# Performance work log

Hardware: AMD Instinct MI355X
Metric: run time of the kernel (lower is better)

## Reference

```python
import jax, jax.numpy as jnp
import numpy as np

# Config constants (mirroring repo globals C.*)
B, L, D = 128, 200, 256          # batch, history length, d_model
NT = 10000                        # num_types (items)
NU = 50000                        # C.USER_NUMBER
NL = 4                            # n_layers
BETA_1 = 0.1                      # C.BETA_1


def _l2norm(x, eps):
    n = jnp.linalg.norm(x, axis=-1, keepdims=True)
    return x / jnp.maximum(n, eps)


def setup_inputs() -> dict:
    key = jax.random.key(0)
    ks = jax.random.split(key, 7)
    user_id = jax.random.randint(ks[0], (B,), 1, NU)
    event_type = jax.random.randint(ks[1], (B, L), 1, NT + 1)  # 1..NT (non-pad)
    adjacent_matrix = jax.random.uniform(ks[2], (NT, NT), jnp.float32)
    pop_encoding = jax.random.normal(ks[3], (NT + 1, D), jnp.float32) * 0.02
    event_emb_w = (jax.random.normal(ks[4], (NT + 1, D), jnp.float32) * 0.02).at[0].set(0.0)
    user_emb_w = (jax.random.normal(ks[5], (NU, D), jnp.float32) * 0.02).at[0].set(0.0)
    layer_ws = jax.random.normal(ks[6], (NL, D, D), jnp.float32) * 0.05
    return {"user_id": user_id, "event_type": event_type,
            "adjacent_matrix": adjacent_matrix, "pop_encoding": pop_encoding,
            "event_emb_w": event_emb_w, "user_emb_w": user_emb_w,
            "layer_ws": layer_ws}


def reference(user_id, event_type, adjacent_matrix, pop_encoding,
              event_emb_w, user_emb_w, layer_ws):
    # non-pad mask (pad idx = 0)
    non_pad = (event_type != 0).astype(jnp.float32)[..., None]  # (B,L,1)

    enc = event_emb_w[event_type]                 # (B,L,D)
    user = user_emb_w[user_id]                    # (B,D)
    pop = pop_encoding[event_type] * non_pad      # (B,L,D)

    # user-specific disentanglement: enc += sign(enc) * normalize(user)
    enc = enc + jnp.sign(enc) * _l2norm(user, 1e-12)[:, None, :]

    # batched adjacency gather: adj[b] = A[e-1][:, e-1] + A[e-1, e-1] (row-broadcast)
    idx = event_type - 1                          # (B,L)
    adj = adjacent_matrix[idx[:, :, None], idx[:, None, :]]      # (B,L,L)
    adj = adj + adjacent_matrix[idx, idx][:, None, :]            # diag broadcast over rows

    # hGCN layer stack: x <- leaky_relu((adj @ x) @ W)
    for i in range(NL):
        enc = jax.nn.leaky_relu(jnp.einsum('bls,bsd->bld', adj, enc) @ layer_ws[i])

    output = enc.mean(axis=1)                     # (B,D)
    user_embeddings = jnp.concatenate([output, pop.mean(axis=1) * BETA_1], axis=-1)  # (B,2D)

    # Predictor (evaluation=True path)
    item_encoding = event_emb_w[1:]               # (NT,D)
    out = user_embeddings[:, :D] @ item_encoding.T  # (B,NT)
    out = _l2norm(out, 1e-5)
    prediction = jnp.tanh(out)
    return prediction, user_embeddings, pop
```

## Files before the change

### kernel.cpp

```cpp
#include <hip/hip_runtime.h>
#include <math.h>

#define B_ 128
#define L_ 200
#define D_ 256
#define NT_ 10000
#define NL_ 4
#define BETA1 0.1f

typedef _Float16 f16x8 __attribute__((ext_vector_type(8)));
typedef _Float16 f16x4 __attribute__((ext_vector_type(4)));
typedef _Float16 f16x2 __attribute__((ext_vector_type(2)));
typedef float f32x4 __attribute__((ext_vector_type(4)));

__device__ __forceinline__ void split2(float v, _Float16& h, _Float16& l) {
    h = (_Float16)v;
    l = (_Float16)(v - (float)h);
}

struct HL { _Float16 h, l; };
__device__ __forceinline__ HL split2v(float v) {
    HL r;
    r.h = (_Float16)v;
    r.l = (_Float16)(v - (float)r.h);
    return r;
}

__device__ __forceinline__ float getscale(const unsigned int* amax, int i, int extra) {
    float am = fmaxf(__uint_as_float(amax[i]), 1e-30f);
    return scalbnf(1.f, 6 - ilogbf(am) - extra);
}

__global__ void user_norm_kernel(const int* __restrict__ user_id,
                                 const float* __restrict__ user_emb_w,
                                 float* __restrict__ unorm,
                                 unsigned int* __restrict__ amax) {
    int b = blockIdx.x;
    int d = threadIdx.x;
    if (b == 0 && d < 16) amax[d] = 0u;
    int uid = user_id[b];
    float v = user_emb_w[(long)uid * D_ + d];
    float sq = v * v;
    for (int off = 32; off > 0; off >>= 1) sq += __shfl_down(sq, off, 64);
    __shared__ float s[4];
    int wid = d >> 6, lane = d & 63;
    if (lane == 0) s[wid] = sq;
    __syncthreads();
    float n = sqrtf(s[0] + s[1] + s[2] + s[3]);
    n = fmaxf(n, 1e-12f);
    unorm[b * D_ + d] = v / n;
}

__global__ void enc0pop_kernel(const int* __restrict__ event_type,
                               const float* __restrict__ E,
                               const float* __restrict__ pope,
                               const float* __restrict__ unorm,
                               float* __restrict__ encF,
                               float* __restrict__ pop_out,
                               unsigned int* __restrict__ amax) {
    int d = threadIdx.x;
    float m = 0.f;
    for (int bl = blockIdx.x; bl < B_ * L_; bl += gridDim.x) {
        int b = bl / L_;
        int et = event_type[bl];
        float e = E[(long)et * D_ + d];
        float sg = (e > 0.f) ? 1.f : ((e < 0.f) ? -1.f : 0.f);
        float u = unorm[b * D_ + d];
        float v = e + sg * u;
        encF[(long)bl * D_ + d] = v;
        m = fmaxf(m, fabsf(v));
        pop_out[(long)bl * D_ + d] = (et != 0) ? pope[(long)et * D_ + d] : 0.f;
    }
    for (int off = 32; off > 0; off >>= 1) m = fmaxf(m, __shfl_down(m, off, 64));
    __shared__ float sm[4];
    int wid = d >> 6, lane = d & 63;
    if (lane == 0) sm[wid] = m;
    __syncthreads();
    if (d == 0)
        atomicMax(amax, __float_as_uint(fmaxf(fmaxf(sm[0], sm[1]), fmaxf(sm[2], sm[3]))));
}

__global__ void diag_kernel(const int* __restrict__ event_type,
                            const float* __restrict__ A,
                            float* __restrict__ diag) {
    int i = blockIdx.x * blockDim.x + threadIdx.x;
    if (i >= B_ * L_) return;
    long idx = (long)event_type[i] - 1;
    diag[i] = A[idx * NT_ + idx];
}

__global__ void adj_split_kernel(const int* __restrict__ event_type,
                                 const float* __restrict__ A,
                                 const float* __restrict__ diag,
                                 _Float16* __restrict__ adjH,
                                 _Float16* __restrict__ adjL) {
    int b = blockIdx.y;
    int i0 = blockIdx.x * 4;
    int j = threadIdx.x;
    __shared__ int sidx[L_];
    __shared__ float sdiag[L_];
    if (j < L_) {
        sidx[j]  = event_type[b * L_ + j] - 1;
        sdiag[j] = diag[b * L_ + j];
    }
    __syncthreads();
    if (j >= L_) return;
    float dj = sdiag[j];
    int cj = sidx[j];
#pragma unroll
    for (int r = 0; r < 4; r++) {
        int i = i0 + r;
        float v = A[(long)sidx[i] * NT_ + cj] + dj;
        HL s = split2v(v);
        long o = ((long)b * L_ + i) * L_ + j;
        adjH[o] = s.h; adjL[o] = s.l;
    }
}

__global__ void wsplit_kernel(const float* __restrict__ W,
                              _Float16* __restrict__ WTh,
                              _Float16* __restrict__ WTl) {
    int layer = blockIdx.z;
    int k0 = blockIdx.y * 64, n0 = blockIdx.x * 64;
    const float* Wl = W + (long)layer * D_ * D_;
    __shared__ float t[64][65];
    int tid = threadIdx.x;
    for (int i = 0; i < 16; i++) {
        int idx = i * 256 + tid;
        int k = idx >> 6, n = idx & 63;
        t[k][n] = Wl[(long)(k0 + k) * D_ + n0 + n];
    }
    __syncthreads();
    for (int i = 0; i < 16; i++) {
        int idx = i * 256 + tid;
        int n = idx >> 6, k = idx & 63;
        float v = t[k][n];
        long o = (long)layer * D_ * D_ + (long)(n0 + n) * D_ + (k0 + k);
        _Float16 h, l;
        split2(v, h, l);
        WTh[o] = h; WTl[o] = l;
    }
}

__global__ void esplit_kernel(const float* __restrict__ E,
                              _Float16* __restrict__ ETh,
                              _Float16* __restrict__ ETl) {
    long f = ((long)blockIdx.x * 256 + threadIdx.x) * 4;
    float4 v = *(const float4*)(E + D_ + f);
    f16x4 h, l;
    HL r0 = split2v(v.x); h[0] = r0.h; l[0] = r0.l;
    HL r1 = split2v(v.y); h[1] = r1.h; l[1] = r1.l;
    HL r2 = split2v(v.z); h[2] = r2.h; l[2] = r2.l;
    HL r3 = split2v(v.w); h[3] = r3.h; l[3] = r3.l;
    *(f16x4*)(ETh + f) = h;
    *(f16x4*)(ETl + f) = l;
}

__global__ __launch_bounds__(256) void gemm1_kernel(
    const _Float16* __restrict__ adjH, const _Float16* __restrict__ adjL,
    const float* __restrict__ encF,
    _Float16* __restrict__ tmpH, _Float16* __restrict__ tmpL,
    const unsigned int* __restrict__ amax, int layer) {
    int b = blockIdx.z;
    const _Float16* Ah = adjH + (long)b * L_ * L_;
    const _Float16* Al = adjL + (long)b * L_ * L_;
    const float*    Bf = encF + (long)b * L_ * D_;
    int m0 = blockIdx.y * 128, n0 = blockIdx.x * 128;
    int tid = threadIdx.x, lane = tid & 63, wid = tid >> 6;
    int wr = wid >> 1, wc = wid & 1;
    float scale = getscale(amax, layer, 0);

    __shared__ _Float16 sAh[128][40], sAl[128][40];
    __shared__ _Float16 sBh[128][40], sBl[128][40];

    f32x4 acc[4][4] = {};
    int fr = lane & 15, kb = (lane >> 4) * 8, fq = lane >> 4;
    int nst = tid & 127, kkst = tid >> 7;

    for (int k0 = 0; k0 < L_; k0 += 32) {
#pragma unroll
        for (int c = 0; c < 2; c++) {
            int idx = c * 256 + tid;
            int row = idx >> 2, kq = (idx & 3) * 8;
            int gk = k0 + kq;
            f16x8 vh = {}, vl = {};
            if (m0 + row < L_ && gk < L_) {
                long o = (long)(m0 + row) * L_ + gk;
                vh = *(const f16x8*)(Ah + o);
                vl = *(const f16x8*)(Al + o);
            }
            *(f16x8*)&sAh[row][kq] = vh;
            *(f16x8*)&sAl[row][kq] = vl;
        }
#pragma unroll
        for (int it = 0; it < 8; it++) {
            int k = kkst * 16 + it * 2;
            int gk0 = k0 + k;
            float v0 = (gk0     < L_) ? Bf[(long)gk0 * D_ + n0 + nst] * scale : 0.f;
            float v1 = (gk0 + 1 < L_) ? Bf[(long)(gk0 + 1) * D_ + n0 + nst] * scale : 0.f;
            f16x2 h, l;
            HL r0 = split2v(v0); h[0] = r0.h; l[0] = r0.l;
            HL r1 = split2v(v1); h[1] = r1.h; l[1] = r1.l;
            int kx = k ^ ((nst & 3) << 3);
            *(f16x2*)&sBh[nst][kx] = h;
            *(f16x2*)&sBl[nst][kx] = l;
        }
        __syncthreads();

        f16x8 fbh[4], fbl[4];
#pragma unroll
        for (int n = 0; n < 4; n++) {
            int rB = wc * 64 + n * 16 + fr;
            int kbB = kb ^ ((rB & 3) << 3);
            fbh[n] = *(const f16x8*)&sBh[rB][kbB];
            fbl[n] = *(const f16x8*)&sBl[rB][kbB];
        }
#pragma unroll
        for (int m = 0; m < 4; m++) {
            int rA = wr * 64 + m * 16 + fr;
            f16x8 fah = *(const f16x8*)&sAh[rA][kb];
            f16x8 fal = *(const f16x8*)&sAl[rA][kb];
#pragma unroll
            for (int n = 0; n < 4; n++) {
                acc[m][n] = __builtin_amdgcn_mfma_f32_16x16x32_f16(fah, fbh[n], acc[m][n], 0, 0, 0);
                acc[m][n] = __builtin_amdgcn_mfma_f32_16x16x32_f16(fah, fbl[n], acc[m][n], 0, 0, 0);
                acc[m][n] = __builtin_amdgcn_mfma_f32_16x16x32_f16(fal, fbh[n], acc[m][n], 0, 0, 0);
            }
        }
        __syncthreads();
    }

    _Float16* Ch = tmpH + (long)b * L_ * D_;
    _Float16* Cl = tmpL + (long)b * L_ * D_;
#pragma unroll
    for (int m = 0; m < 4; m++)
#pragma unroll
        for (int n = 0; n < 4; n++)
#pragma unroll
            for (int r = 0; r < 4; r++) {
                int row = m0 + wr * 64 + m * 16 + fq * 4 + r;
                int col = n0 + wc * 64 + n * 16 + fr;
                if (row < L_) {
                    float v = acc[m][n][r];
                    HL s = split2v(v);
                    long o = (long)row * D_ + col;
                    Ch[o] = s.h; Cl[o] = s.l;
                }
            }
}

__global__ __launch_bounds__(256) void gemm2_kernel(
    const _Float16* __restrict__ Ah, const _Float16* __restrict__ Al,
    const _Float16* __restrict__ Bh, const _Float16* __restrict__ Bl,
    float* __restrict__ Cf, unsigned int* __restrict__ amax) {
    int m0 = blockIdx.y * 128, n0 = blockIdx.x * 128;
    int tid = threadIdx.x, lane = tid & 63, wid = tid >> 6;
    int wr = wid >> 1, wc = wid & 1;
    __shared__ _Float16 sAh[128][40], sAl[128][40];
    __shared__ _Float16 sBh[128][40], sBl[128][40];
    __shared__ float sRed[4];
    f32x4 acc[4][4] = {};
    int fr = lane & 15, kb = (lane >> 4) * 8, fq = lane >> 4;

    for (int k0 = 0; k0 < D_; k0 += 32) {
#pragma unroll
        for (int c = 0; c < 2; c++) {
            int idx = c * 256 + tid;
            int row = idx >> 2, kq = (idx & 3) * 8, gk = k0 + kq;
            long oa = (long)(m0 + row) * D_ + gk;
            *(f16x8*)&sAh[row][kq] = *(const f16x8*)(Ah + oa);
            *(f16x8*)&sAl[row][kq] = *(const f16x8*)(Al + oa);
            long ob = (long)(n0 + row) * D_ + gk;
            *(f16x8*)&sBh[row][kq] = *(const f16x8*)(Bh + ob);
            *(f16x8*)&sBl[row][kq] = *(const f16x8*)(Bl + ob);
        }
        __syncthreads();
        f16x8 fbh[4], fbl[4];
#pragma unroll
        for (int n = 0; n < 4; n++) {
            int rB = wc * 64 + n * 16 + fr;
            fbh[n] = *(const f16x8*)&sBh[rB][kb];
            fbl[n] = *(const f16x8*)&sBl[rB][kb];
        }
#pragma unroll
        for (int m = 0; m < 4; m++) {
            int rA = wr * 64 + m * 16 + fr;
            f16x8 fah = *(const f16x8*)&sAh[rA][kb];
            f16x8 fal = *(const f16x8*)&sAl[rA][kb];
#pragma unroll
            for (int n = 0; n < 4; n++) {
                acc[m][n] = __builtin_amdgcn_mfma_f32_16x16x32_f16(fah, fbh[n], acc[m][n], 0, 0, 0);
                acc[m][n] = __builtin_amdgcn_mfma_f32_16x16x32_f16(fah, fbl[n], acc[m][n], 0, 0, 0);
                acc[m][n] = __builtin_amdgcn_mfma_f32_16x16x32_f16(fal, fbh[n], acc[m][n], 0, 0, 0);
            }
        }
        __syncthreads();
    }

    float tmax = 0.f;
#pragma unroll
    for (int m = 0; m < 4; m++)
#pragma unroll
        for (int n = 0; n < 4; n++)
#pragma unroll
            for (int r = 0; r < 4; r++) {
                int row = m0 + wr * 64 + m * 16 + fq * 4 + r;
                int col = n0 + wc * 64 + n * 16 + fr;
                float v = acc[m][n][r];
                v = (v >= 0.f) ? v : 0.01f * v;
                Cf[(long)row * D_ + col] = v;
                tmax = fmaxf(tmax, fabsf(v));
            }
    for (int off = 32; off > 0; off >>= 1) tmax = fmaxf(tmax, __shfl_down(tmax, off, 64));
    if (lane == 0) sRed[wid] = tmax;
    __syncthreads();
    if (tid == 0)
        atomicMax(amax, __float_as_uint(fmaxf(fmaxf(sRed[0], sRed[1]), fmaxf(sRed[2], sRed[3]))));
}

__global__ __launch_bounds__(1024) void mean_fused_kernel(
    const float* __restrict__ encF,
    const int* __restrict__ event_type,
    const float* __restrict__ pope,
    const unsigned int* __restrict__ amax,
    float* __restrict__ ue,
    _Float16* __restrict__ ueh,
    _Float16* __restrict__ uel) {
    int b = blockIdx.x, tid = threadIdx.x;
    int c = tid >> 8, d = tid & 255;
    float s1 = 0.f, s2 = 0.f;
    int l0 = c * 50;
    for (int l = l0; l < l0 + 50; l++) {
        s1 += encF[((long)b * L_ + l) * D_ + d];
        int et = event_type[b * L_ + l];
        s2 += (et != 0) ? pope[(long)et * D_ + d] : 0.f;
    }
    __shared__ float red1[4][256], red2[4][256];
    red1[c][d] = s1;
    red2[c][d] = s2;
    __syncthreads();
    if (c == 0) {
        s1 = red1[0][d] + red1[1][d] + red1[2][d] + red1[3][d];
        s2 = red2[0][d] + red2[1][d] + red2[2][d] + red2[3][d];
        float S = 1.f;
        for (int i = 0; i < NL_; i++) S *= getscale(amax, i, 0);
        ue[b * 2 * D_ + d]      = s1 / (float)L_ / S;
        ue[b * 2 * D_ + D_ + d] = s2 * (BETA1 / (float)L_);
        float sc = getscale(amax, NL_, 8);
        HL r = split2v(s1 * sc);
        ueh[b * D_ + d] = r.h;
        uel[b * D_ + d] = r.l;
    }
}

__global__ __launch_bounds__(256) void pred_mfma_kernel(
    const _Float16* __restrict__ Ah, const _Float16* __restrict__ Al,
    const _Float16* __restrict__ Bh, const _Float16* __restrict__ Bl,
    float* __restrict__ Cf) {
    int n0 = blockIdx.x * 64;
    int tid = threadIdx.x, lane = tid & 63, wid = tid >> 6;
    int wr = wid >> 1, wc = wid & 1;
    __shared__ _Float16 sAh[128][40], sAl[128][40];
    __shared__ _Float16 sBh[64][40], sBl[64][40];
    f32x4 acc[4][2] = {};
    int fr = lane & 15, kb = (lane >> 4) * 8, fq = lane >> 4;

    for (int k0 = 0; k0 < D_; k0 += 32) {
#pragma unroll
        for (int c = 0; c < 2; c++) {
            int idx = c * 256 + tid;
            int row = idx >> 2, kq = (idx & 3) * 8, gk = k0 + kq;
            long oa = (long)row * D_ + gk;
            *(f16x8*)&sAh[row][kq] = *(const f16x8*)(Ah + oa);
            *(f16x8*)&sAl[row][kq] = *(const f16x8*)(Al + oa);
        }
        {
            int row = tid >> 2, kq = (tid & 3) * 8, gk = k0 + kq;
            f16x8 wh = {}, wl = {};
            if (n0 + row < NT_) {
                long ob = (long)(n0 + row) * D_ + gk;
                wh = *(const f16x8*)(Bh + ob);
                wl = *(const f16x8*)(Bl + ob);
            }
            *(f16x8*)&sBh[row][kq] = wh;
            *(f16x8*)&sBl[row][kq] = wl;
        }
        __syncthreads();
        f16x8 fbh[2], fbl[2];
#pragma unroll
        for (int n = 0; n < 2; n++) {
            int rB = wc * 32 + n * 16 + fr;
            fbh[n] = *(const f16x8*)&sBh[rB][kb];
            fbl[n] = *(const f16x8*)&sBl[rB][kb];
        }
#pragma unroll
        for (int m = 0; m < 4; m++) {
            int rA = wr * 64 + m * 16 + fr;
            f16x8 fah = *(const f16x8*)&sAh[rA][kb];
            f16x8 fal = *(const f16x8*)&sAl[rA][kb];
#pragma unroll
            for (int n = 0; n < 2; n++) {
                acc[m][n] = __builtin_amdgcn_mfma_f32_16x16x32_f16(fah, fbh[n], acc[m][n], 0, 0, 0);
                acc[m][n] = __builtin_amdgcn_mfma_f32_16x16x32_f16(fah, fbl[n], acc[m][n], 0, 0, 0);
                acc[m][n] = __builtin_amdgcn_mfma_f32_16x16x32_f16(fal, fbh[n], acc[m][n], 0, 0, 0);
            }
        }
        __syncthreads();
    }
#pragma unroll
    for (int m = 0; m < 4; m++)
#pragma unroll
        for (int n = 0; n < 2; n++)
#pragma unroll
            for (int r = 0; r < 4; r++) {
                int row = wr * 64 + m * 16 + fq * 4 + r;
                int col = n0 + wc * 32 + n * 16 + fr;
                if (col < NT_)
                    Cf[(long)row * NT_ + col] = acc[m][n][r];
            }
}

__global__ void normtanh2_kernel(float* __restrict__ pred) {
    int b = blockIdx.x, t = threadIdx.x;
    float* row = pred + (long)b * NT_;
    float v[10];
    float sq = 0.f;
#pragma unroll
    for (int p = 0; p < 10; p++) {
        int i = p * 1024 + t;
        v[p] = (i < NT_) ? row[i] : 0.f;
        sq += v[p] * v[p];
    }
    for (int off = 32; off > 0; off >>= 1) sq += __shfl_down(sq, off, 64);
    __shared__ float s[16];
    if ((t & 63) == 0) s[t >> 6] = sq;
    __syncthreads();
    float n = 0.f;
    for (int i = 0; i < 16; i++) n += s[i];
    float inv = 1.f / fmaxf(sqrtf(n), 1e-5f);
#pragma unroll
    for (int p = 0; p < 10; p++) {
        int i = p * 1024 + t;
        if (i < NT_) row[i] = tanhf(v[p] * inv);
    }
}

__global__ void enc0_kernel(const int* __restrict__ event_type,
                            const float* __restrict__ E,
                            const float* __restrict__ unorm,
                            float* __restrict__ encF) {
    int d = threadIdx.x;
    for (int bl = blockIdx.x; bl < B_ * L_; bl += gridDim.x) {
        int b = bl / L_;
        int et = event_type[bl];
        float e = E[(long)et * D_ + d];
        float sg = (e > 0.f) ? 1.f : ((e < 0.f) ? -1.f : 0.f);
        float u = unorm[b * D_ + d];
        encF[(long)bl * D_ + d] = e + sg * u;
    }
}

__global__ void pop_kernel(const int* __restrict__ event_type,
                           const float* __restrict__ pope,
                           float* __restrict__ pop_out) {
    int bl = blockIdx.x;
    int d = threadIdx.x;
    int et = event_type[bl];
    float np = (et != 0) ? 1.0f : 0.0f;
    pop_out[(long)bl * D_ + d] = pope[(long)et * D_ + d] * np;
}

template <bool BT, bool LEAKY>
__global__ void gemm_kernel(const float* __restrict__ A,
                            const float* __restrict__ Bm,
                            float* __restrict__ C,
                            int M, int N, int K, int lda, int ldb, int ldc,
                            long strideA, long strideB, long strideC) {
    int batch = blockIdx.z;
    A  += (long)batch * strideA;
    Bm += (long)batch * strideB;
    C  += (long)batch * strideC;
    const int BM = 64, BN = 64, BK = 16;
    __shared__ float As[BK][BM + 1];
    __shared__ float Bs[BK][BN + 1];
    int tid = threadIdx.x;
    int m0 = blockIdx.y * BM, n0 = blockIdx.x * BN;
    int tx = tid & 15, ty = tid >> 4;
    float acc[4][4] = {};
    for (int k0 = 0; k0 < K; k0 += BK) {
        {
            int m = tid >> 2, kk = (tid & 3) * 4;
            int gm = m0 + m;
#pragma unroll
            for (int q = 0; q < 4; q++) {
                int gk = k0 + kk + q;
                float x = (gm < M && gk < K) ? A[(long)gm * lda + gk] : 0.f;
                As[kk + q][m] = x;
            }
        }
        if (!BT) {
            int kk = tid >> 4, n = (tid & 15) * 4;
            int gk = k0 + kk;
#pragma unroll
            for (int q = 0; q < 4; q++) {
                int gn = n0 + n + q;
                float x = (gk < K && gn < N) ? Bm[(long)gk * ldb + gn] : 0.f;
                Bs[kk][n + q] = x;
            }
        } else {
            int n = tid >> 2, kk = (tid & 3) * 4;
            int gn = n0 + n;
#pragma unroll
            for (int q = 0; q < 4; q++) {
                int gk = k0 + kk + q;
                float x = (gn < N && gk < K) ? Bm[(long)gn * ldb + gk] : 0.f;
                Bs[kk + q][n] = x;
            }
        }
        __syncthreads();
#pragma unroll
        for (int kk = 0; kk < BK; kk++) {
            float a[4], bv[4];
#pragma unroll
            for (int q = 0; q < 4; q++) a[q] = As[kk][ty * 4 + q];
#pragma unroll
            for (int q = 0; q < 4; q++) bv[q] = Bs[kk][tx * 4 + q];
#pragma unroll
            for (int i = 0; i < 4; i++)
#pragma unroll
                for (int j = 0; j < 4; j++)
                    acc[i][j] += a[i] * bv[j];
        }
        __syncthreads();
    }
#pragma unroll
    for (int i = 0; i < 4; i++) {
        int gm = m0 + ty * 4 + i;
        if (gm >= M) continue;
#pragma unroll
        for (int j = 0; j < 4; j++) {
            int gn = n0 + tx * 4 + j;
            if (gn >= N) continue;
            float v = acc[i][j];
            if (LEAKY) v = (v >= 0.f) ? v : 0.01f * v;
            C[(long)gm * ldc + gn] = v;
        }
    }
}

__global__ void mean_plain_kernel(const float* __restrict__ enc,
                                  const int* __restrict__ event_type,
                                  const float* __restrict__ pope,
                                  float* __restrict__ ue) {
    int b = blockIdx.x, d = threadIdx.x;
    float s1 = 0.f, s2 = 0.f;
    for (int l = 0; l < L_; l++) {
        s1 += enc[((long)b * L_ + l) * D_ + d];
        int et = event_type[b * L_ + l];
        float np = (et != 0) ? 1.0f : 0.0f;
        s2 += pope[(long)et * D_ + d] * np;
    }
    ue[b * (2 * D_) + d]      = s1 / (float)L_;
    ue[b * (2 * D_) + D_ + d] = (s2 / (float)L_) * BETA1;
}

__global__ void adj_kernel_f32(const int* __restrict__ event_type,
                               const float* __restrict__ A,
                               const float* __restrict__ diag,
                               float* __restrict__ adj) {
    int b = blockIdx.y;
    int i = blockIdx.x;
    int j = threadIdx.x;
    __shared__ int sidx[L_];
    __shared__ float sdiag[L_];
    if (j < L_) {
        sidx[j]  = event_type[b * L_ + j] - 1;
        sdiag[j] = diag[b * L_ + j];
    }
    __syncthreads();
    if (j >= L_) return;
    long row = (long)event_type[b * L_ + i] - 1;
    adj[((long)b * L_ + i) * L_ + j] = A[row * NT_ + sidx[j]] + sdiag[j];
}

__global__ void normtanh_kernel(float* __restrict__ pred) {
    int b = blockIdx.x;
    int t = threadIdx.x;
    float* row = pred + (long)b * NT_;
    float sq = 0.f;
    for (int i = t; i < NT_; i += 256) { float v = row[i]; sq += v * v; }
    for (int off = 32; off > 0; off >>= 1) sq += __shfl_down(sq, off, 64);
    __shared__ float s[4];
    int wid = t >> 6, lane = t & 63;
    if (lane == 0) s[wid] = sq;
    __syncthreads();
    float n = sqrtf(s[0] + s[1] + s[2] + s[3]);
    n = fmaxf(n, 1e-5f);
    float inv = 1.f / n;
    for (int i = t; i < NT_; i += 256) row[i] = tanhf(row[i] * inv);
}

extern "C" void kernel_launch(void* const* d_in, const int* in_sizes, int n_in,
                              void* d_out, int out_size, void* d_ws, size_t ws_size,
                              hipStream_t stream) {
    const int*   user_id    = (const int*)d_in[0];
    const int*   event_type = (const int*)d_in[1];
    const float* A          = (const float*)d_in[2];
    const float* pope       = (const float*)d_in[3];
    const float* E          = (const float*)d_in[4];
    const float* U          = (const float*)d_in[5];
    const float* W          = (const float*)d_in[6];

    float* out  = (float*)d_out;
    float* pred = out;
    float* ue   = out + (long)B_ * NT_;
    float* pop  = ue  + (long)B_ * 2 * D_;

    char* w = (char*)d_ws;
    auto carve = [&](size_t bytes) { char* p = w; w += (bytes + 255) & ~(size_t)255; return p; };
    unsigned int* amax = (unsigned int*)carve(64);
    _Float16* adjH  = (_Float16*)carve((size_t)B_ * L_ * L_ * 2);
    _Float16* adjL  = (_Float16*)carve((size_t)B_ * L_ * L_ * 2);
    _Float16* tmpH  = (_Float16*)carve((size_t)B_ * L_ * D_ * 2);
    _Float16* tmpL  = (_Float16*)carve((size_t)B_ * L_ * D_ * 2);
    float*    encF  = (float*)carve((size_t)B_ * L_ * D_ * 4);
    _Float16* WTh   = (_Float16*)carve((size_t)NL_ * D_ * D_ * 2);
    _Float16* WTl   = (_Float16*)carve((size_t)NL_ * D_ * D_ * 2);
    _Float16* ETh   = (_Float16*)carve((size_t)NT_ * D_ * 2);
    _Float16* ETl   = (_Float16*)carve((size_t)NT_ * D_ * 2);
    _Float16* ueh   = (_Float16*)carve((size_t)B_ * D_ * 2);
    _Float16* uel   = (_Float16*)carve((size_t)B_ * D_ * 2);
    float*    unorm = (float*)carve((size_t)B_ * D_ * 4);
    float*    diag  = (float*)carve((size_t)B_ * L_ * 4);
    size_t needed = (size_t)(w - (char*)d_ws);

    if (ws_size >= needed) {
        user_norm_kernel<<<B_, 256, 0, stream>>>(user_id, U, unorm, amax);
        enc0pop_kernel<<<1280, 256, 0, stream>>>(event_type, E, pope, unorm, encF, pop, amax);
        diag_kernel<<<(B_ * L_ + 255) / 256, 256, 0, stream>>>(event_type, A, diag);
        adj_split_kernel<<<dim3(50, B_), 256, 0, stream>>>(event_type, A, diag, adjH, adjL);
        wsplit_kernel<<<dim3(4, 4, NL_), 256, 0, stream>>>(W, WTh, WTl);
        esplit_kernel<<<NT_ * D_ / 1024, 256, 0, stream>>>(E, ETh, ETl);

        for (int i = 0; i < NL_; i++) {
            gemm1_kernel<<<dim3(2, 2, B_), 256, 0, stream>>>(
                adjH, adjL, encF, tmpH, tmpL, amax, i);
            gemm2_kernel<<<dim3(2, B_ * L_ / 128), 256, 0, stream>>>(
                tmpH, tmpL, WTh + (long)i * D_ * D_, WTl + (long)i * D_ * D_,
                encF, amax + i + 1);
        }

        mean_fused_kernel<<<B_, 1024, 0, stream>>>(encF, event_type, pope, amax, ue, ueh, uel);
        pred_mfma_kernel<<<(NT_ + 63) / 64, 256, 0, stream>>>(ueh, uel, ETh, ETl, pred);
        normtanh2_kernel<<<B_, 1024, 0, stream>>>(pred);
    } else {
        float* ws0   = (float*)d_ws;
        float* uno   = ws0;
        float* dia   = uno + B_ * D_;
        float* adjF  = dia + B_ * L_;
        float* encA2 = adjF + (long)B_ * L_ * L_;
        float* encB2 = encA2 + (long)B_ * L_ * D_;
        float* tmp   = pop;

        user_norm_kernel<<<B_, 256, 0, stream>>>(user_id, U, uno, (unsigned int*)dia);
        enc0_kernel<<<1280, 256, 0, stream>>>(event_type, E, uno, encA2);
        diag_kernel<<<(B_ * L_ + 255) / 256, 256, 0, stream>>>(event_type, A, dia);
        adj_kernel_f32<<<dim3(L_, B_), 256, 0, stream>>>(event_type, A, dia, adjF);

        float* cur = encA2; float* nxt = encB2;
        for (int i = 0; i < NL_; i++) {
            dim3 g1((D_ + 63) / 64, (L_ + 63) / 64, B_);
            gemm_kernel<false, false><<<g1, 256, 0, stream>>>(
                adjF, cur, tmp, L_, D_, L_, L_, D_, D_,
                (long)L_ * L_, (long)L_ * D_, (long)L_ * D_);
            dim3 g2((D_ + 63) / 64, (B_ * L_ + 63) / 64, 1);
            gemm_kernel<false, true><<<g2, 256, 0, stream>>>(
                tmp, W + (long)i * D_ * D_, nxt, B_ * L_, D_, D_, D_, D_, D_, 0, 0, 0);
            float* t = cur; cur = nxt; nxt = t;
        }
        pop_kernel<<<B_ * L_, 256, 0, stream>>>(event_type, pope, pop);
        mean_plain_kernel<<<B_, 256, 0, stream>>>(cur, event_type, pope, ue);

        dim3 g3((NT_ + 63) / 64, (B_ + 63) / 64, 1);
        gemm_kernel<true, false><<<g3, 256, 0, stream>>>(
            ue, E + D_, pred, B_, NT_, D_, 2 * D_, D_, NT_, 0, 0, 0);
        normtanh_kernel<<<B_, 256, 0, stream>>>(pred);
    }
}
```

Before: 425.7 us.

## Pre-split and transpose encodings into padded fp16 buffers before the adjacency GEMM

A new per-layer kernel scales the fp32 encodings, splits them into high and low fp16 parts, and writes them transposed into a zero-padded (D x 224) layout. The adjacency GEMM can then load its B operand with vector loads instead of doing strided scalar fp32 loads and splitting inside the GEMM. Shared-memory row padding also changes from 40 to 36 halves, with fragment loads split into 8-byte halves, to alter the bank-conflict pattern. The cost is an extra launch per layer and an extra write and read of the split encoding buffers.

```diff
diff --git a/kernel.cpp b/kernel.cpp
--- a/kernel.cpp
+++ b/kernel.cpp
@@ -3,6 +3,7 @@
 
 #define B_ 128
 #define L_ 200
+#define LP_ 224
 #define D_ 256
 #define NT_ 10000
 #define NL_ 4
@@ -10,13 +11,7 @@
 
 typedef _Float16 f16x8 __attribute__((ext_vector_type(8)));
 typedef _Float16 f16x4 __attribute__((ext_vector_type(4)));
-typedef _Float16 f16x2 __attribute__((ext_vector_type(2)));
 typedef float f32x4 __attribute__((ext_vector_type(4)));
-
-__device__ __forceinline__ void split2(float v, _Float16& h, _Float16& l) {
-    h = (_Float16)v;
-    l = (_Float16)(v - (float)h);
-}
 
 struct HL { _Float16 h, l; };
 __device__ __forceinline__ HL split2v(float v) {
@@ -29,6 +24,22 @@
 __device__ __forceinline__ float getscale(const unsigned int* amax, int i, int extra) {
     float am = fmaxf(__uint_as_float(amax[i]), 1e-30f);
     return scalbnf(1.f, 6 - ilogbf(am) - extra);
+}
+
+__device__ __forceinline__ f16x8 ld8(const _Float16* p) {
+    f16x4 a = *(const f16x4*)p;
+    f16x4 b = *(const f16x4*)(p + 4);
+    f16x8 r;
+    r[0] = a[0]; r[1] = a[1]; r[2] = a[2]; r[3] = a[3];
+    r[4] = b[0]; r[5] = b[1]; r[6] = b[2]; r[7] = b[3];
+    return r;
+}
+__device__ __forceinline__ void st8(_Float16* p, f16x8 v) {
+    f16x4 a, b;
+    a[0] = v[0]; a[1] = v[1]; a[2] = v[2]; a[3] = v[3];
+    b[0] = v[4]; b[1] = v[5]; b[2] = v[6]; b[3] = v[7];
+    *(f16x4*)p = a;
+    *(f16x4*)(p + 4) = b;
 }
 
 __global__ void user_norm_kernel(const int* __restrict__ user_id,
@@ -136,9 +147,8 @@
         int n = idx >> 6, k = idx & 63;
         float v = t[k][n];
         long o = (long)layer * D_ * D_ + (long)(n0 + n) * D_ + (k0 + k);
-        _Float16 h, l;
-        split2(v, h, l);
-        WTh[o] = h; WTl[o] = l;
+        HL r = split2v(v);
+        WTh[o] = r.h; WTl[o] = r.l;
     }
 }
 
@@ -156,28 +166,54 @@
     *(f16x4*)(ETl + f) = l;
 }
 
+__global__ void split_enc_kernel(const float* __restrict__ encF,
+                                 _Float16* __restrict__ Th,
+                                 _Float16* __restrict__ Tl,
+                                 const unsigned int* __restrict__ amax, int layer) {
+    int b = blockIdx.z;
+    int l0 = blockIdx.y * 64, d0 = blockIdx.x * 64;
+    float scale = getscale(amax, layer, 0);
+    __shared__ float t[64][65];
+    int tid = threadIdx.x;
+    for (int i = 0; i < 16; i++) {
+        int idx = i * 256 + tid;
+        int l = idx >> 6, d = idx & 63;
+        float v = (l0 + l < L_) ? encF[((long)b * L_ + l0 + l) * D_ + d0 + d] * scale : 0.f;
+        t[l][d] = v;
+    }
+    __syncthreads();
+    for (int i = 0; i < 16; i++) {
+        int idx = i * 256 + tid;
+        int d = idx >> 6, l = idx & 63;
+        int gl = l0 + l;
+        if (gl < LP_) {
+            HL r = split2v(t[l][d]);
+            long o = ((long)b * D_ + d0 + d) * LP_ + gl;
+            Th[o] = r.h; Tl[o] = r.l;
+        }
+    }
+}
+
 __global__ __launch_bounds__(256) void gemm1_kernel(
     const _Float16* __restrict__ adjH, const _Float16* __restrict__ adjL,
-    const float* __restrict__ encF,
-    _Float16* __restrict__ tmpH, _Float16* __restrict__ tmpL,
-    const unsigned int* __restrict__ amax, int layer) {
+    const _Float16* __restrict__ encTh, const _Float16* __restrict__ encTl,
+    _Float16* __restrict__ tmpH, _Float16* __restrict__ tmpL) {
     int b = blockIdx.z;
     const _Float16* Ah = adjH + (long)b * L_ * L_;
     const _Float16* Al = adjL + (long)b * L_ * L_;
-    const float*    Bf = encF + (long)b * L_ * D_;
+    const _Float16* Bh = encTh + (long)b * D_ * LP_;
+    const _Float16* Bl = encTl + (long)b * D_ * LP_;
     int m0 = blockIdx.y * 128, n0 = blockIdx.x * 128;
     int tid = threadIdx.x, lane = tid & 63, wid = tid >> 6;
     int wr = wid >> 1, wc = wid & 1;
-    float scale = getscale(amax, layer, 0);
-
-    __shared__ _Float16 sAh[128][40], sAl[128][40];
-    __shared__ _Float16 sBh[128][40], sBl[128][40];
+
+    __shared__ alignas(16) _Float16 sAh[128][36], sAl[128][36];
+    __shared__ alignas(16) _Float16 sBh[128][36], sBl[128][36];
 
     f32x4 acc[4][4] = {};
     int fr = lane & 15, kb = (lane >> 4) * 8, fq = lane >> 4;
-    int nst = tid & 127, kkst = tid >> 7;
-
-    for (int k0 = 0; k0 < L_; k0 += 32) {
+
+    for (int k0 = 0; k0 < LP_; k0 += 32) {
 #pragma unroll
         for (int c = 0; c < 2; c++) {
             int idx = c * 256 + tid;
@@ -189,21 +225,11 @@
                 vh = *(const f16x8*)(Ah + o);
                 vl = *(const f16x8*)(Al + o);
             }
-            *(f16x8*)&sAh[row][kq] = vh;
-            *(f16x8*)&sAl[row][kq] = vl;
-        }
-#pragma unroll
-        for (int it = 0; it < 8; it++) {
-            int k = kkst * 16 + it * 2;
-            int gk0 = k0 + k;
-            float v0 = (gk0     < L_) ? Bf[(long)gk0 * D_ + n0 + nst] * scale : 0.f;
-            float v1 = (gk0 + 1 < L_) ? Bf[(long)(gk0 + 1) * D_ + n0 + nst] * scale : 0.f;
-            f16x2 h, l;
-            HL r0 = split2v(v0); h[0] = r0.h; l[0] = r0.l;
-            HL r1 = split2v(v1); h[1] = r1.h; l[1] = r1.l;
-            int kx = k ^ ((nst & 3) << 3);
-            *(f16x2*)&sBh[nst][kx] = h;
-            *(f16x2*)&sBl[nst][kx] = l;
+            st8(&sAh[row][kq], vh);
+            st8(&sAl[row][kq], vl);
+            long ob = (long)(n0 + row) * LP_ + gk;
+            st8(&sBh[row][kq], *(const f16x8*)(Bh + ob));
+            st8(&sBl[row][kq], *(const f16x8*)(Bl + ob));
         }
         __syncthreads();
 
@@ -211,15 +237,14 @@
 #pragma unroll
         for (int n = 0; n < 4; n++) {
             int rB = wc * 64 + n * 16 + fr;
-            int kbB = kb ^ ((rB & 3) << 3);
-            fbh[n] = *(const f16x8*)&sBh[rB][kbB];
-            fbl[n] = *(const f16x8*)&sBl[rB][kbB];
+            fbh[n] = ld8(&sBh[rB][kb]);
+            fbl[n] = ld8(&sBl[rB][kb]);
         }
 #pragma unroll
         for (int m = 0; m < 4; m++) {
             int rA = wr * 64 + m * 16 + fr;
-            f16x8 fah = *(const f16x8*)&sAh[rA][kb];
-            f16x8 fal = *(const f16x8*)&sAl[rA][kb];
+            f16x8 fah = ld8(&sAh[rA][kb]);
+            f16x8 fal = ld8(&sAl[rA][kb]);
 #pragma unroll
             for (int n = 0; n < 4; n++) {
                 acc[m][n] = __builtin_amdgcn_mfma_f32_16x16x32_f16(fah, fbh[n], acc[m][n], 0, 0, 0);
@@ -241,8 +266,7 @@
                 int row = m0 + wr * 64 + m * 16 + fq * 4 + r;
                 int col = n0 + wc * 64 + n * 16 + fr;
                 if (row < L_) {
-                    float v = acc[m][n][r];
-                    HL s = split2v(v);
+                    HL s = split2v(acc[m][n][r]);
                     long o = (long)row * D_ + col;
                     Ch[o] = s.h; Cl[o] = s.l;
                 }
@@ -256,8 +280,8 @@
     int m0 = blockIdx.y * 128, n0 = blockIdx.x * 128;
     int tid = threadIdx.x, lane = tid & 63, wid = tid >> 6;
     int wr = wid >> 1, wc = wid & 1;
-    __shared__ _Float16 sAh[128][40], sAl[128][40];
-    __shared__ _Float16 sBh[128][40], sBl[128][40];
+    __shared__ alignas(16) _Float16 sAh[128][36], sAl[128][36];
+    __shared__ alignas(16) _Float16 sBh[128][36], sBl[128][36];
     __shared__ float sRed[4];
     f32x4 acc[4][4] = {};
     int fr = lane & 15, kb = (lane >> 4) * 8, fq = lane >> 4;
@@ -268,25 +292,25 @@
             int idx = c * 256 + tid;
             int row = idx >> 2, kq = (idx & 3) * 8, gk = k0 + kq;
             long oa = (long)(m0 + row) * D_ + gk;
-            *(f16x8*)&sAh[row][kq] = *(const f16x8*)(Ah + oa);
-            *(f16x8*)&sAl[row][kq] = *(const f16x8*)(Al + oa);
+            st8(&sAh[row][kq], *(const f16x8*)(Ah + oa));
+            st8(&sAl[row][kq], *(const f16x8*)(Al + oa));
             long ob = (long)(n0 + row) * D_ + gk;
-            *(f16x8*)&sBh[row][kq] = *(const f16x8*)(Bh + ob);
-            *(f16x8*)&sBl[row][kq] = *(const f16x8*)(Bl + ob);
+            st8(&sBh[row][kq], *(const f16x8*)(Bh + ob));
+            st8(&sBl[row][kq], *(const f16x8*)(Bl + ob));
         }
         __syncthreads();
         f16x8 fbh[4], fbl[4];
 #pragma unroll
         for (int n = 0; n < 4; n++) {
             int rB = wc * 64 + n * 16 + fr;
-            fbh[n] = *(const f16x8*)&sBh[rB][kb];
-            fbl[n] = *(const f16x8*)&sBl[rB][kb];
+            fbh[n] = ld8(&sBh[rB][kb]);
+            fbl[n] = ld8(&sBl[rB][kb]);
         }
 #pragma unroll
         for (int m = 0; m < 4; m++) {
             int rA = wr * 64 + m * 16 + fr;
-            f16x8 fah = *(const f16x8*)&sAh[rA][kb];
-            f16x8 fal = *(const f16x8*)&sAl[rA][kb];
+            f16x8 fah = ld8(&sAh[rA][kb]);
+            f16x8 fal = ld8(&sAl[rA][kb]);
 #pragma unroll
             for (int n = 0; n < 4; n++) {
                 acc[m][n] = __builtin_amdgcn_mfma_f32_16x16x32_f16(fah, fbh[n], acc[m][n], 0, 0, 0);
@@ -360,8 +384,8 @@
     int n0 = blockIdx.x * 64;
     int tid = threadIdx.x, lane = tid & 63, wid = tid >> 6;
     int wr = wid >> 1, wc = wid & 1;
-    __shared__ _Float16 sAh[128][40], sAl[128][40];
-    __shared__ _Float16 sBh[64][40], sBl[64][40];
+    __shared__ alignas(16) _Float16 sAh[128][36], sAl[128][36];
+    __shared__ alignas(16) _Float16 sBh[64][36], sBl[64][36];
     f32x4 acc[4][2] = {};
     int fr = lane & 15, kb = (lane >> 4) * 8, fq = lane >> 4;
 
@@ -371,8 +395,8 @@
             int idx = c * 256 + tid;
             int row = idx >> 2, kq = (idx & 3) * 8, gk = k0 + kq;
             long oa = (long)row * D_ + gk;
-            *(f16x8*)&sAh[row][kq] = *(const f16x8*)(Ah + oa);
-            *(f16x8*)&sAl[row][kq] = *(const f16x8*)(Al + oa);
+            st8(&sAh[row][kq], *(const f16x8*)(Ah + oa));
+            st8(&sAl[row][kq], *(const f16x8*)(Al + oa));
         }
         {
             int row = tid >> 2, kq = (tid & 3) * 8, gk = k0 + kq;
@@ -382,22 +406,22 @@
                 wh = *(const f16x8*)(Bh + ob);
                 wl = *(const f16x8*)(Bl + ob);
             }
-            *(f16x8*)&sBh[row][kq] = wh;
-            *(f16x8*)&sBl[row][kq] = wl;
+            st8(&sBh[row][kq], wh);
+            st8(&sBl[row][kq], wl);
         }
         __syncthreads();
         f16x8 fbh[2], fbl[2];
 #pragma unroll
         for (int n = 0; n < 2; n++) {
             int rB = wc * 32 + n * 16 + fr;
-            fbh[n] = *(const f16x8*)&sBh[rB][kb];
-            fbl[n] = *(const f16x8*)&sBl[rB][kb];
+            fbh[n] = ld8(&sBh[rB][kb]);
+            fbl[n] = ld8(&sBl[rB][kb]);
         }
 #pragma unroll
         for (int m = 0; m < 4; m++) {
             int rA = wr * 64 + m * 16 + fr;
-            f16x8 fah = *(const f16x8*)&sAh[rA][kb];
-            f16x8 fal = *(const f16x8*)&sAl[rA][kb];
+            f16x8 fah = ld8(&sAh[rA][kb]);
+            f16x8 fal = ld8(&sAl[rA][kb]);
 #pragma unroll
             for (int n = 0; n < 2; n++) {
                 acc[m][n] = __builtin_amdgcn_mfma_f32_16x16x32_f16(fah, fbh[n], acc[m][n], 0, 0, 0);
@@ -621,6 +645,8 @@
     unsigned int* amax = (unsigned int*)carve(64);
     _Float16* adjH  = (_Float16*)carve((size_t)B_ * L_ * L_ * 2);
     _Float16* adjL  = (_Float16*)carve((size_t)B_ * L_ * L_ * 2);
+    _Float16* encTh = (_Float16*)carve((size_t)B_ * D_ * LP_ * 2);
+    _Float16* encTl = (_Float16*)carve((size_t)B_ * D_ * LP_ * 2);
     _Float16* tmpH  = (_Float16*)carve((size_t)B_ * L_ * D_ * 2);
     _Float16* tmpL  = (_Float16*)carve((size_t)B_ * L_ * D_ * 2);
     float*    encF  = (float*)carve((size_t)B_ * L_ * D_ * 4);
@@ -643,8 +669,9 @@
         esplit_kernel<<<NT_ * D_ / 1024, 256, 0, stream>>>(E, ETh, ETl);
 
         for (int i = 0; i < NL_; i++) {
+            split_enc_kernel<<<dim3(4, 4, B_), 256, 0, stream>>>(encF, encTh, encTl, amax, i);
             gemm1_kernel<<<dim3(2, 2, B_), 256, 0, stream>>>(
-                adjH, adjL, encF, tmpH, tmpL, amax, i);
+                adjH, adjL, encTh, encTl, tmpH, tmpL);
             gemm2_kernel<<<dim3(2, B_ * L_ / 128), 256, 0, stream>>>(
                 tmpH, tmpL, WTh + (long)i * D_ * D_, WTl + (long)i * D_ * D_,
                 encF, amax + i + 1);
```

New measurement: 450.6 us. +5.8%, slower.
